# Kernel tuning notes

Measured on AMD Instinct MI355X. Metric: run time of the kernel, lower is better.

Reference implementation:

```python
import jax, jax.numpy as jnp
import numpy as np

# ---- configuration mirrored from init_kwargs ----
NUM_TREES = 8
NUM_NODES = 5
C = 16          # in_channels
B, H, W = 8, 224, 224
SEED = 0
NEG = -1e30     # maxplus semiring zero (avoid -inf for fp16/bf16 safety)


def make_forest():
    """Random recursive trees: node 0 is the root, parent[i] < i."""
    rng = np.random.default_rng(SEED)
    parents = []
    for _ in range(NUM_TREES):
        p = [-1] + [int(rng.integers(0, i)) for i in range(1, NUM_NODES)]
        parents.append(p)
    return parents


def excl_prefix_max(v):
    """Strict 2D prefix max: out[h,w] = max over h'<h, w'<w of v[h',w'].
    Semiring 'cumulative sum' (maxplus add = max) with exclusive shift."""
    c = jax.lax.cummax(jax.lax.cummax(v, axis=2), axis=3)
    c = c[:, :, :-1, :-1]
    return jnp.pad(c, ((0, 0), (0, 0), (1, 0), (1, 0)), constant_values=NEG)


def setup_inputs() -> dict:
    key = jax.random.key(0)
    kx, ka = jax.random.split(key)
    x = jax.random.normal(kx, (B, C, H, W), dtype=jnp.float32)
    alphas = jax.random.normal(ka, (NUM_TREES, NUM_NODES, C), dtype=jnp.float32)
    return {"x": x, "alphas": alphas}


def reference(x, alphas):
    parents = make_forest()  # static structure (seed-fixed)
    # valuate: map to log domain for the maxplus semiring
    xv = jnp.log1p(jax.nn.relu(x))  # [B, C, H, W]

    outs = []
    for t in range(NUM_TREES):
        par = parents[t]
        acc = [None] * NUM_NODES   # maxplus-product (= +) of children prefix maxes
        root_val = None
        # bottom-up over nodes (parent index < child index)
        for i in range(NUM_NODES - 1, -1, -1):
            # maxplus scaling by alpha: alpha + x
            v = xv + alphas[t, i][None, :, None, None]
            if acc[i] is not None:
                v = v + acc[i]          # semiring product with children
            if i > 0:
                s = excl_prefix_max(v)  # semiring cumulative over quadrant
                p = par[i]
                acc[p] = s if acc[p] is None else acc[p] + s
            else:
                root_val = v
        # root aggregation: maxplus sum over all pixels -> [B, C]
        outs.append(jnp.max(root_val, axis=(2, 3)))
    res = jnp.stack(outs, axis=1)  # [B, NUM_TREES, C]
    # devaluate: back from log domain
    return jnp.expm1(res)
```

## Files before the change

kernel.cpp:

```cpp
#include <hip/hip_runtime.h>
#include <stdint.h>

#define NTREES 8
#define NNODES 5
#define CC 16
#define BB 8
#define HH 224
#define WW 224
#define NBAND 28

struct Forest { int par[NTREES * NNODES]; };
struct Cls { int v[NTREES]; };

namespace nprng {

struct Pcg {
  __uint128_t state, inc;
  int has_uint32;
  uint32_t uinteger;
};

static inline __uint128_t pcg_mult() {
  return (((__uint128_t)0x2360ED051FC65DA4ULL) << 64) | 0x4385DF649FCCF645ULL;
}

static inline void pcg_step(Pcg& s) { s.state = s.state * pcg_mult() + s.inc; }

static inline uint64_t pcg_next64(Pcg& s) {
  pcg_step(s);
  uint64_t xored = (uint64_t)(s.state >> 64) ^ (uint64_t)s.state;
  unsigned rot = (unsigned)(s.state >> 122);
  return (xored >> rot) | (xored << ((64u - rot) & 63u));
}

static inline uint32_t pcg_next32(Pcg& s) {
  if (s.has_uint32) { s.has_uint32 = 0; return s.uinteger; }
  uint64_t n = pcg_next64(s);
  s.has_uint32 = 1;
  s.uinteger = (uint32_t)(n >> 32);
  return (uint32_t)n;
}

static inline uint32_t lemire32(Pcg& s, uint32_t rng) {
  const uint32_t rng_excl = rng + 1u;
  uint64_t m = (uint64_t)pcg_next32(s) * (uint64_t)rng_excl;
  uint32_t leftover = (uint32_t)m;
  if (leftover < rng_excl) {
    const uint32_t threshold = (uint32_t)((0xFFFFFFFFu - rng) % rng_excl);
    while (leftover < threshold) {
      m = (uint64_t)pcg_next32(s) * (uint64_t)rng_excl;
      leftover = (uint32_t)m;
    }
  }
  return (uint32_t)(m >> 32);
}

static void make_forest(Forest& f) {
  const uint32_t INIT_A = 0x43b0d7e5u, MULT_A = 0x931e8875u;
  const uint32_t INIT_B = 0x8b51f9ddu, MULT_B = 0x58f38dedu;
  const uint32_t MIX_L  = 0xca01f9ddu, MIX_R  = 0x4973f715u;
  uint32_t pool[4];
  uint32_t hc = INIT_A;
  auto hashmix = [&](uint32_t v) -> uint32_t {
    v ^= hc; hc *= MULT_A; v *= hc; v ^= v >> 16; return v;
  };
  auto mix = [&](uint32_t x, uint32_t y) -> uint32_t {
    uint32_t r = MIX_L * x - MIX_R * y; r ^= r >> 16; return r;
  };
  pool[0] = hashmix(0u);
  for (int i = 1; i < 4; ++i) pool[i] = hashmix(0u);
  for (int is = 0; is < 4; ++is)
    for (int id = 0; id < 4; ++id)
      if (is != id) pool[id] = mix(pool[id], hashmix(pool[is]));
  uint32_t st32[8];
  uint32_t hb = INIT_B;
  for (int i = 0; i < 8; ++i) {
    uint32_t dv = pool[i & 3];
    dv ^= hb; hb *= MULT_B; dv *= hb; dv ^= dv >> 16;
    st32[i] = dv;
  }
  uint64_t w64[4];
  for (int i = 0; i < 4; ++i)
    w64[i] = (uint64_t)st32[2 * i] | ((uint64_t)st32[2 * i + 1] << 32);

  __uint128_t initstate = (((__uint128_t)w64[0]) << 64) | w64[1];
  __uint128_t initseq   = (((__uint128_t)w64[2]) << 64) | w64[3];
  Pcg s;
  s.state = 0; s.inc = (initseq << 1) | 1;
  pcg_step(s);
  s.state += initstate;
  pcg_step(s);
  s.has_uint32 = 0; s.uinteger = 0;

  for (int t = 0; t < NTREES; ++t) {
    f.par[t * NNODES + 0] = -1;
    for (int i = 1; i < NNODES; ++i) {
      uint32_t rng = (uint32_t)(i - 1);
      f.par[t * NNODES + i] = (rng == 0) ? 0 : (int)lemire32(s, rng);
    }
  }
}

}

static int classify_tree(const int* p) {
  int nch[NNODES] = {0, 0, 0, 0, 0};
  for (int i = 1; i < NNODES; ++i) nch[p[i]]++;
  int internals[3], nI = 0;
  for (int i = 1; i <= 3; ++i) if (nch[i] > 0) internals[nI++] = i;
  if (nI == 0) return 1;
  if (nI == 1) {
    int m = nch[internals[0]];
    return m == 1 ? 2 : (m == 2 ? 3 : 4);
  }
  if (nI == 2) {
    int i = internals[0], j = internals[1];
    if (p[j] == i) {
      if (nch[j] == 2) return 9;
      return (nch[i] - 1 == 1) ? 7 : 6;
    }
    return 5;
  }
  return 8;
}

template <int CL> struct TC;
template <> struct TC<1> { static constexpr int H1=0,E1L=0,H2=0,E2L=0,H3=0,RL=4,R1=0,R2=0,R3=0; };
template <> struct TC<2> { static constexpr int H1=1,E1L=1,H2=0,E2L=0,H3=0,RL=2,R1=1,R2=0,R3=0; };
template <> struct TC<3> { static constexpr int H1=1,E1L=2,H2=0,E2L=0,H3=0,RL=1,R1=1,R2=0,R3=0; };
template <> struct TC<4> { static constexpr int H1=1,E1L=3,H2=0,E2L=0,H3=0,RL=0,R1=1,R2=0,R3=0; };
template <> struct TC<5> { static constexpr int H1=1,E1L=1,H2=0,E2L=0,H3=0,RL=0,R1=2,R2=0,R3=0; };
template <> struct TC<6> { static constexpr int H1=1,E1L=1,H2=1,E2L=0,H3=0,RL=1,R1=0,R2=1,R3=0; };
template <> struct TC<7> { static constexpr int H1=1,E1L=1,H2=1,E2L=1,H3=0,RL=0,R1=0,R2=1,R3=0; };
template <> struct TC<8> { static constexpr int H1=1,E1L=1,H2=1,E2L=0,H3=1,RL=0,R1=0,R2=0,R3=1; };
template <> struct TC<9> { static constexpr int H1=1,E1L=2,H2=1,E2L=0,H3=0,RL=0,R1=0,R2=1,R3=0; };

__device__ __forceinline__ float wshr1(float t) {
  int r = __builtin_amdgcn_update_dpp(
      0, __builtin_bit_cast(int, t), 0x138, 0xf, 0xf, true);
  return __builtin_bit_cast(float, r);
}

#define S8STAGE(MODS) \
  "v_max_f32_dpp %0, %0, %0 " MODS "\n\t" \
  "v_max_f32_dpp %1, %1, %1 " MODS "\n\t" \
  "v_max_f32_dpp %2, %2, %2 " MODS "\n\t" \
  "v_max_f32_dpp %3, %3, %3 " MODS "\n\t" \
  "v_max_f32_dpp %4, %4, %4 " MODS "\n\t" \
  "v_max_f32_dpp %5, %5, %5 " MODS "\n\t" \
  "v_max_f32_dpp %6, %6, %6 " MODS "\n\t" \
  "v_max_f32_dpp %7, %7, %7 " MODS "\n\t"

#define SCAN8(q)                                              \
  asm volatile(                                               \
      "s_nop 1\n\t"                                           \
      S8STAGE("row_shr:1 row_mask:0xf bank_mask:0xf")         \
      S8STAGE("row_shr:2 row_mask:0xf bank_mask:0xf")         \
      S8STAGE("row_shr:4 row_mask:0xf bank_mask:0xf")         \
      S8STAGE("row_shr:8 row_mask:0xf bank_mask:0xf")         \
      S8STAGE("row_bcast:15 row_mask:0xa bank_mask:0xf")      \
      S8STAGE("row_bcast:31 row_mask:0xc bank_mask:0xf")      \
      "s_nop 1"                                               \
      : "+v"(q[0]), "+v"(q[1]), "+v"(q[2]), "+v"(q[3]),       \
        "+v"(q[4]), "+v"(q[5]), "+v"(q[6]), "+v"(q[7]))

#define MUL4(d, s) { (d).x *= (s).x; (d).y *= (s).y; (d).z *= (s).z; (d).w *= (s).w; }
#define MAX4(d, s) { (d).x = fmaxf((d).x,(s).x); (d).y = fmaxf((d).y,(s).y); \
                     (d).z = fmaxf((d).z,(s).z); (d).w = fmaxf((d).w,(s).w); }

template <int E>
__device__ __forceinline__ void powmul(float4& v, const float4& s) {
  if constexpr (E == 4) {
    float4 t = s; MUL4(t, t); MUL4(t, t); MUL4(v, t);
  } else {
    if constexpr (E >= 1) MUL4(v, s);
    if constexpr (E >= 2) MUL4(v, s);
    if constexpr (E >= 3) MUL4(v, s);
  }
}

__device__ __forceinline__ float4 shiftrow(const float4* M, int u, const float4& carry) {
  float4 p = (u == 0) ? carry : M[u - 1];
  return make_float4(wshr1(p.w), p.x, p.y, p.z);
}

template <int CL>
__device__ __forceinline__ void run_tree(const float* __restrict__ cp,
                                         float mask, float asum,
                                         float* __restrict__ outp, int lane) {
  using F = TC<CL>;
  const float4 z4 = make_float4(0.f, 0.f, 0.f, 0.f);
  float4 cL = z4, c1 = z4, c2 = z4, c3 = z4, racc = z4;

  float4 X[8];
#pragma unroll
  for (int u = 0; u < 8; ++u) X[u] = *(const float4*)(cp + u * WW);

#pragma unroll 1
  for (int band = 0; band < NBAND; ++band) {
    const int nb = (band + 1 < NBAND) ? band + 1 : NBAND - 1;
    float4 T[8];
#pragma unroll
    for (int u = 0; u < 8; ++u)
      T[u] = *(const float4*)(cp + (size_t)(nb * 8 + u) * WW);

    float4 fv[8];
#pragma unroll
    for (int u = 0; u < 8; ++u) {
      const float4 xr = X[u];
      fv[u].x = fmaf(fmaxf(xr.x, 0.f), mask, mask);
      fv[u].y = fmaf(fmaxf(xr.y, 0.f), mask, mask);
      fv[u].z = fmaf(fmaxf(xr.z, 0.f), mask, mask);
      fv[u].w = fmaf(fmaxf(xr.w, 0.f), mask, mask);
    }

    float4 ML[8], M1[8], M2[8], M3[8];

    {
      float l0[8], l1[8], l2[8], q[8];
#pragma unroll
      for (int u = 0; u < 8; ++u) {
        l0[u] = fv[u].x;
        l1[u] = fmaxf(l0[u], fv[u].y);
        l2[u] = fmaxf(l1[u], fv[u].z);
        q[u]  = fmaxf(l2[u], fv[u].w);
      }
      SCAN8(q);
      float4 run = cL;
#pragma unroll
      for (int u = 0; u < 8; ++u) {
        float e = wshr1(q[u]);
        run.x = fmaxf(run.x, fmaxf(e, l0[u]));
        run.y = fmaxf(run.y, fmaxf(e, l1[u]));
        run.z = fmaxf(run.z, fmaxf(e, l2[u]));
        run.w = fmaxf(run.w, q[u]);
        ML[u] = run;
      }
    }

    if constexpr (F::H1) {
      float l0[8], l1[8], l2[8], q[8];
#pragma unroll
      for (int u = 0; u < 8; ++u) {
        float4 v = fv[u];
        powmul<F::E1L>(v, shiftrow(ML, u, cL));
        l0[u] = v.x;
        l1[u] = fmaxf(l0[u], v.y);
        l2[u] = fmaxf(l1[u], v.z);
        q[u]  = fmaxf(l2[u], v.w);
      }
      SCAN8(q);
      float4 run = c1;
#pragma unroll
      for (int u = 0; u < 8; ++u) {
        float e = wshr1(q[u]);
        run.x = fmaxf(run.x, fmaxf(e, l0[u]));
        run.y = fmaxf(run.y, fmaxf(e, l1[u]));
        run.z = fmaxf(run.z, fmaxf(e, l2[u]));
        run.w = fmaxf(run.w, q[u]);
        M1[u] = run;
      }
    }

    if constexpr (F::H2) {
      float l0[8], l1[8], l2[8], q[8];
#pragma unroll
      for (int u = 0; u < 8; ++u) {
        float4 v = fv[u];
        if constexpr (F::E2L > 0) powmul<F::E2L>(v, shiftrow(ML, u, cL));
        { float4 s1 = shiftrow(M1, u, c1); MUL4(v, s1); }
        l0[u] = v.x;
        l1[u] = fmaxf(l0[u], v.y);
        l2[u] = fmaxf(l1[u], v.z);
        q[u]  = fmaxf(l2[u], v.w);
      }
      SCAN8(q);
      float4 run = c2;
#pragma unroll
      for (int u = 0; u < 8; ++u) {
        float e = wshr1(q[u]);
        run.x = fmaxf(run.x, fmaxf(e, l0[u]));
        run.y = fmaxf(run.y, fmaxf(e, l1[u]));
        run.z = fmaxf(run.z, fmaxf(e, l2[u]));
        run.w = fmaxf(run.w, q[u]);
        M2[u] = run;
      }
    }

    if constexpr (F::H3) {
      float l0[8], l1[8], l2[8], q[8];
#pragma unroll
      for (int u = 0; u < 8; ++u) {
        float4 v = fv[u];
        { float4 s2 = shiftrow(M2, u, c2); MUL4(v, s2); }
        l0[u] = v.x;
        l1[u] = fmaxf(l0[u], v.y);
        l2[u] = fmaxf(l1[u], v.z);
        q[u]  = fmaxf(l2[u], v.w);
      }
      SCAN8(q);
      float4 run = c3;
#pragma unroll
      for (int u = 0; u < 8; ++u) {
        float e = wshr1(q[u]);
        run.x = fmaxf(run.x, fmaxf(e, l0[u]));
        run.y = fmaxf(run.y, fmaxf(e, l1[u]));
        run.z = fmaxf(run.z, fmaxf(e, l2[u]));
        run.w = fmaxf(run.w, q[u]);
        M3[u] = run;
      }
    }

#pragma unroll
    for (int u = 0; u < 8; ++u) {
      float4 r = fv[u];
      if constexpr (F::RL > 0) powmul<F::RL>(r, shiftrow(ML, u, cL));
      if constexpr (F::R1 > 0) powmul<F::R1>(r, shiftrow(M1, u, c1));
      if constexpr (F::R2 > 0) powmul<F::R2>(r, shiftrow(M2, u, c2));
      if constexpr (F::R3 > 0) powmul<F::R3>(r, shiftrow(M3, u, c3));
      MAX4(racc, r);
    }

    cL = ML[7];
    if constexpr (F::H1) c1 = M1[7];
    if constexpr (F::H2) c2 = M2[7];
    if constexpr (F::H3) c3 = M3[7];

#pragma unroll
    for (int u = 0; u < 8; ++u) X[u] = T[u];
  }

  float m = fmaxf(fmaxf(racc.x, racc.y), fmaxf(racc.z, racc.w));
#pragma unroll
  for (int d = 1; d < 64; d <<= 1) m = fmaxf(m, __shfl_xor(m, d));
  if (lane == 0) *outp = expf(asum) * m - 1.f;
}

__global__ __launch_bounds__(64) void fis_kernel(const float* __restrict__ x,
                                                 const float* __restrict__ alphas,
                                                 float* __restrict__ out,
                                                 Cls cls) {
  const int lane = threadIdx.x;
  const int blk  = blockIdx.x;
  const int t    = blk >> 7;
  const int bc   = blk & 127;
  const int c    = bc & (CC - 1);
  const int b    = bc >> 4;

  const float* __restrict__ xp = x + (size_t)bc * (HH * WW);

  float asum = 0.f;
#pragma unroll
  for (int i = 0; i < NNODES; ++i) asum += alphas[(t * NNODES + i) * CC + c];

  const int   w0   = lane * 4;
  const float mask = (w0 < WW) ? 1.0f : 0.0f;
  const float* __restrict__ cp = xp + ((w0 < WW) ? w0 : (WW - 4));
  float* outp = out + ((size_t)b * NTREES + t) * CC + c;

  switch (cls.v[t]) {
    case 1: run_tree<1>(cp, mask, asum, outp, lane); break;
    case 2: run_tree<2>(cp, mask, asum, outp, lane); break;
    case 3: run_tree<3>(cp, mask, asum, outp, lane); break;
    case 4: run_tree<4>(cp, mask, asum, outp, lane); break;
    case 5: run_tree<5>(cp, mask, asum, outp, lane); break;
    case 6: run_tree<6>(cp, mask, asum, outp, lane); break;
    case 7: run_tree<7>(cp, mask, asum, outp, lane); break;
    case 8: run_tree<8>(cp, mask, asum, outp, lane); break;
    case 9: run_tree<9>(cp, mask, asum, outp, lane); break;
    default: break;
  }
}

extern "C" void kernel_launch(void* const* d_in, const int* in_sizes, int n_in,
                              void* d_out, int out_size, void* d_ws, size_t ws_size,
                              hipStream_t stream) {
  const float* x      = (const float*)d_in[0];
  const float* alphas = (const float*)d_in[1];
  float* out          = (float*)d_out;

  Forest f;
  nprng::make_forest(f);

  Cls cls;
  for (int t = 0; t < NTREES; ++t)
    cls.v[t] = classify_tree(&f.par[t * NNODES]);

  dim3 grid(BB * CC * NTREES);
  dim3 block(64);
  hipLaunchKernelGGL(fis_kernel, grid, block, 0, stream, x, alphas, out, cls);
}
```

Baseline: 98.31 us.

## Halve row band height and compute exclusive prefix scan directly

Each loop iteration now processes 4 rows instead of 8, so there are twice as many bands. The scan routine now emits the exclusive (shifted) prefix max directly, which removes the separate shiftrow step and its extra DPP shift per consumer. Both changes cut register pressure and the DPP shift work. The trade-off is more loop iterations with less instruction-level parallelism per DPP scan stage, and shorter load batches per band.

Result: slower. 100.3 us (+2.0%).

```diff
diff --git a/kernel.cpp b/kernel.cpp
--- a/kernel.cpp
+++ b/kernel.cpp
@@ -7,7 +7,7 @@
 #define BB 8
 #define HH 224
 #define WW 224
-#define NBAND 28
+#define NBAND 56
 
 struct Forest { int par[NTREES * NNODES]; };
 struct Cls { int v[NTREES]; };
@@ -141,28 +141,23 @@
   return __builtin_bit_cast(float, r);
 }
 
-#define S8STAGE(MODS) \
+#define S4STAGE(MODS) \
   "v_max_f32_dpp %0, %0, %0 " MODS "\n\t" \
   "v_max_f32_dpp %1, %1, %1 " MODS "\n\t" \
   "v_max_f32_dpp %2, %2, %2 " MODS "\n\t" \
-  "v_max_f32_dpp %3, %3, %3 " MODS "\n\t" \
-  "v_max_f32_dpp %4, %4, %4 " MODS "\n\t" \
-  "v_max_f32_dpp %5, %5, %5 " MODS "\n\t" \
-  "v_max_f32_dpp %6, %6, %6 " MODS "\n\t" \
-  "v_max_f32_dpp %7, %7, %7 " MODS "\n\t"
-
-#define SCAN8(q)                                              \
+  "v_max_f32_dpp %3, %3, %3 " MODS "\n\t"
+
+#define SCAN4(a, b, c, d)                                     \
   asm volatile(                                               \
       "s_nop 1\n\t"                                           \
-      S8STAGE("row_shr:1 row_mask:0xf bank_mask:0xf")         \
-      S8STAGE("row_shr:2 row_mask:0xf bank_mask:0xf")         \
-      S8STAGE("row_shr:4 row_mask:0xf bank_mask:0xf")         \
-      S8STAGE("row_shr:8 row_mask:0xf bank_mask:0xf")         \
-      S8STAGE("row_bcast:15 row_mask:0xa bank_mask:0xf")      \
-      S8STAGE("row_bcast:31 row_mask:0xc bank_mask:0xf")      \
+      S4STAGE("row_shr:1 row_mask:0xf bank_mask:0xf")         \
+      S4STAGE("row_shr:2 row_mask:0xf bank_mask:0xf")         \
+      S4STAGE("row_shr:4 row_mask:0xf bank_mask:0xf")         \
+      S4STAGE("row_shr:8 row_mask:0xf bank_mask:0xf")         \
+      S4STAGE("row_bcast:15 row_mask:0xa bank_mask:0xf")      \
+      S4STAGE("row_bcast:31 row_mask:0xc bank_mask:0xf")      \
       "s_nop 1"                                               \
-      : "+v"(q[0]), "+v"(q[1]), "+v"(q[2]), "+v"(q[3]),       \
-        "+v"(q[4]), "+v"(q[5]), "+v"(q[6]), "+v"(q[7]))
+      : "+v"(a), "+v"(b), "+v"(c), "+v"(d))
 
 #define MUL4(d, s) { (d).x *= (s).x; (d).y *= (s).y; (d).z *= (s).z; (d).w *= (s).w; }
 #define MAX4(d, s) { (d).x = fmaxf((d).x,(s).x); (d).y = fmaxf((d).y,(s).y); \
@@ -179,9 +174,46 @@
   }
 }
 
-__device__ __forceinline__ float4 shiftrow(const float4* M, int u, const float4& carry) {
-  float4 p = (u == 0) ? carry : M[u - 1];
-  return make_float4(wshr1(p.w), p.x, p.y, p.z);
+__device__ __forceinline__ void scan_pass(const float4 v[4], float4 S[4],
+                                          const float4& carry) {
+  float l1a = fmaxf(v[0].x, v[0].y), l2a = fmaxf(l1a, v[0].z), qa = fmaxf(l2a, v[0].w);
+  float l1b = fmaxf(v[1].x, v[1].y), l2b = fmaxf(l1b, v[1].z), qb = fmaxf(l2b, v[1].w);
+  float l1c = fmaxf(v[2].x, v[2].y), l2c = fmaxf(l1c, v[2].z), qc = fmaxf(l2c, v[2].w);
+  float l1d = fmaxf(v[3].x, v[3].y), l2d = fmaxf(l1d, v[3].z), qd = fmaxf(l2d, v[3].w);
+  SCAN4(qa, qb, qc, qd);
+  float4 run = carry;
+  {
+    float e = wshr1(qa);
+    run.x = fmaxf(run.x, e);
+    run.y = fmaxf(run.y, fmaxf(e, v[0].x));
+    run.z = fmaxf(run.z, fmaxf(e, l1a));
+    run.w = fmaxf(run.w, fmaxf(e, l2a));
+    S[0] = run;
+  }
+  {
+    float e = wshr1(qb);
+    run.x = fmaxf(run.x, e);
+    run.y = fmaxf(run.y, fmaxf(e, v[1].x));
+    run.z = fmaxf(run.z, fmaxf(e, l1b));
+    run.w = fmaxf(run.w, fmaxf(e, l2b));
+    S[1] = run;
+  }
+  {
+    float e = wshr1(qc);
+    run.x = fmaxf(run.x, e);
+    run.y = fmaxf(run.y, fmaxf(e, v[2].x));
+    run.z = fmaxf(run.z, fmaxf(e, l1c));
+    run.w = fmaxf(run.w, fmaxf(e, l2c));
+    S[2] = run;
+  }
+  {
+    float e = wshr1(qd);
+    run.x = fmaxf(run.x, e);
+    run.y = fmaxf(run.y, fmaxf(e, v[3].x));
+    run.z = fmaxf(run.z, fmaxf(e, l1d));
+    run.w = fmaxf(run.w, fmaxf(e, l2d));
+    S[3] = run;
+  }
 }
 
 template <int CL>
@@ -192,21 +224,21 @@
   const float4 z4 = make_float4(0.f, 0.f, 0.f, 0.f);
   float4 cL = z4, c1 = z4, c2 = z4, c3 = z4, racc = z4;
 
-  float4 X[8];
-#pragma unroll
-  for (int u = 0; u < 8; ++u) X[u] = *(const float4*)(cp + u * WW);
+  float4 X[4];
+#pragma unroll
+  for (int u = 0; u < 4; ++u) X[u] = *(const float4*)(cp + u * WW);
 
 #pragma unroll 1
   for (int band = 0; band < NBAND; ++band) {
     const int nb = (band + 1 < NBAND) ? band + 1 : NBAND - 1;
-    float4 T[8];
-#pragma unroll
-    for (int u = 0; u < 8; ++u)
-      T[u] = *(const float4*)(cp + (size_t)(nb * 8 + u) * WW);
-
-    float4 fv[8];
-#pragma unroll
-    for (int u = 0; u < 8; ++u) {
+    float4 T[4];
+#pragma unroll
+    for (int u = 0; u < 4; ++u)
+      T[u] = *(const float4*)(cp + (size_t)(nb * 4 + u) * WW);
+
+    float4 fv[4];
+#pragma unroll
+    for (int u = 0; u < 4; ++u) {
       const float4 xr = X[u];
       fv[u].x = fmaf(fmaxf(xr.x, 0.f), mask, mask);
       fv[u].y = fmaf(fmaxf(xr.y, 0.f), mask, mask);
@@ -214,120 +246,58 @@
       fv[u].w = fmaf(fmaxf(xr.w, 0.f), mask, mask);
     }
 
-    float4 ML[8], M1[8], M2[8], M3[8];
-
-    {
-      float l0[8], l1[8], l2[8], q[8];
-#pragma unroll
-      for (int u = 0; u < 8; ++u) {
-        l0[u] = fv[u].x;
-        l1[u] = fmaxf(l0[u], fv[u].y);
-        l2[u] = fmaxf(l1[u], fv[u].z);
-        q[u]  = fmaxf(l2[u], fv[u].w);
+    float4 SL[4], S1[4], S2[4], S3[4];
+
+    scan_pass(fv, SL, cL);
+
+    if constexpr (F::H1) {
+      float4 v[4];
+#pragma unroll
+      for (int u = 0; u < 4; ++u) {
+        v[u] = fv[u];
+        powmul<F::E1L>(v[u], (u == 0) ? cL : SL[u - 1]);
       }
-      SCAN8(q);
-      float4 run = cL;
-#pragma unroll
-      for (int u = 0; u < 8; ++u) {
-        float e = wshr1(q[u]);
-        run.x = fmaxf(run.x, fmaxf(e, l0[u]));
-        run.y = fmaxf(run.y, fmaxf(e, l1[u]));
-        run.z = fmaxf(run.z, fmaxf(e, l2[u]));
-        run.w = fmaxf(run.w, q[u]);
-        ML[u] = run;
+      scan_pass(v, S1, c1);
+    }
+
+    if constexpr (F::H2) {
+      float4 v[4];
+#pragma unroll
+      for (int u = 0; u < 4; ++u) {
+        v[u] = fv[u];
+        if constexpr (F::E2L > 0) powmul<F::E2L>(v[u], (u == 0) ? cL : SL[u - 1]);
+        { float4 s = (u == 0) ? c1 : S1[u - 1]; MUL4(v[u], s); }
       }
-    }
-
-    if constexpr (F::H1) {
-      float l0[8], l1[8], l2[8], q[8];
-#pragma unroll
-      for (int u = 0; u < 8; ++u) {
-        float4 v = fv[u];
-        powmul<F::E1L>(v, shiftrow(ML, u, cL));
-        l0[u] = v.x;
-        l1[u] = fmaxf(l0[u], v.y);
-        l2[u] = fmaxf(l1[u], v.z);
-        q[u]  = fmaxf(l2[u], v.w);
+      scan_pass(v, S2, c2);
+    }
+
+    if constexpr (F::H3) {
+      float4 v[4];
+#pragma unroll
+      for (int u = 0; u < 4; ++u) {
+        v[u] = fv[u];
+        { float4 s = (u == 0) ? c2 : S2[u - 1]; MUL4(v[u], s); }
       }
-      SCAN8(q);
-      float4 run = c1;
-#pragma unroll
-      for (int u = 0; u < 8; ++u) {
-        float e = wshr1(q[u]);
-        run.x = fmaxf(run.x, fmaxf(e, l0[u]));
-        run.y = fmaxf(run.y, fmaxf(e, l1[u]));
-        run.z = fmaxf(run.z, fmaxf(e, l2[u]));
-        run.w = fmaxf(run.w, q[u]);
-        M1[u] = run;
-      }
-    }
-
-    if constexpr (F::H2) {
-      float l0[8], l1[8], l2[8], q[8];
-#pragma unroll
-      for (int u = 0; u < 8; ++u) {
-        float4 v = fv[u];
-        if constexpr (F::E2L > 0) powmul<F::E2L>(v, shiftrow(ML, u, cL));
-        { float4 s1 = shiftrow(M1, u, c1); MUL4(v, s1); }
-        l0[u] = v.x;
-        l1[u] = fmaxf(l0[u], v.y);
-        l2[u] = fmaxf(l1[u], v.z);
-        q[u]  = fmaxf(l2[u], v.w);
-      }
-      SCAN8(q);
-      float4 run = c2;
-#pragma unroll
-      for (int u = 0; u < 8; ++u) {
-        float e = wshr1(q[u]);
-        run.x = fmaxf(run.x, fmaxf(e, l0[u]));
-        run.y = fmaxf(run.y, fmaxf(e, l1[u]));
-        run.z = fmaxf(run.z, fmaxf(e, l2[u]));
-        run.w = fmaxf(run.w, q[u]);
-        M2[u] = run;
-      }
-    }
-
-    if constexpr (F::H3) {
-      float l0[8], l1[8], l2[8], q[8];
-#pragma unroll
-      for (int u = 0; u < 8; ++u) {
-        float4 v = fv[u];
-        { float4 s2 = shiftrow(M2, u, c2); MUL4(v, s2); }
-        l0[u] = v.x;
-        l1[u] = fmaxf(l0[u], v.y);
-        l2[u] = fmaxf(l1[u], v.z);
-        q[u]  = fmaxf(l2[u], v.w);
-      }
-      SCAN8(q);
-      float4 run = c3;
-#pragma unroll
-      for (int u = 0; u < 8; ++u) {
-        float e = wshr1(q[u]);
-        run.x = fmaxf(run.x, fmaxf(e, l0[u]));
-        run.y = fmaxf(run.y, fmaxf(e, l1[u]));
-        run.z = fmaxf(run.z, fmaxf(e, l2[u]));
-        run.w = fmaxf(run.w, q[u]);
-        M3[u] = run;
-      }
-    }
-
-#pragma unroll
-    for (int u = 0; u < 8; ++u) {
+      scan_pass(v, S3, c3);
+    }
+
+#pragma unroll
+    for (int u = 0; u < 4; ++u) {
       float4 r = fv[u];
-      if constexpr (F::RL > 0) powmul<F::RL>(r, shiftrow(ML, u, cL));
-      if constexpr (F::R1 > 0) powmul<F::R1>(r, shiftrow(M1, u, c1));
-      if constexpr (F::R2 > 0) powmul<F::R2>(r, shiftrow(M2, u, c2));
-      if constexpr (F::R3 > 0) powmul<F::R3>(r, shiftrow(M3, u, c3));
+      if constexpr (F::RL > 0) powmul<F::RL>(r, (u == 0) ? cL : SL[u - 1]);
+      if constexpr (F::R1 > 0) powmul<F::R1>(r, (u == 0) ? c1 : S1[u - 1]);
+      if constexpr (F::R2 > 0) powmul<F::R2>(r, (u == 0) ? c2 : S2[u - 1]);
+      if constexpr (F::R3 > 0) powmul<F::R3>(r, (u == 0) ? c3 : S3[u - 1]);
       MAX4(racc, r);
     }
 
-    cL = ML[7];
-    if constexpr (F::H1) c1 = M1[7];
-    if constexpr (F::H2) c2 = M2[7];
-    if constexpr (F::H3) c3 = M3[7];
-
-#pragma unroll
-    for (int u = 0; u < 8; ++u) X[u] = T[u];
+    cL = SL[3];
+    if constexpr (F::H1) c1 = S1[3];
+    if constexpr (F::H2) c2 = S2[3];
+    if constexpr (F::H3) c3 = S3[3];
+
+#pragma unroll
+    for (int u = 0; u < 4; ++u) X[u] = T[u];
   }
 
   float m = fmaxf(fmaxf(racc.x, racc.y), fmaxf(racc.z, racc.w));
```
